# Kernel tuning notes

Hardware: AMD Instinct MI355X
Metric: run time of the kernel (lower is better)

## Reference

```python
import jax, jax.numpy as jnp
import numpy as np

E = 1024      # embed_dim
H = 16        # num_heads
HD = E // H   # head_dim = 64
WIN = 256     # window_size
LN_EPS = 1e-5


def _layernorm(x, g, b):
    mu = jnp.mean(x, axis=-1, keepdims=True)
    var = jnp.var(x, axis=-1, keepdims=True)
    return (x - mu) * jax.lax.rsqrt(var + LN_EPS) * g + b


def _rope_tables(S):
    freqs = 1.0 / (10000.0 ** (jnp.arange(0, HD, 2, dtype=jnp.float32) / HD))  # [HD/2]
    t = jnp.arange(S, dtype=jnp.float32)
    fr = jnp.outer(t, freqs)                      # [S, HD/2]
    emb = jnp.concatenate([fr, fr], axis=-1)      # [S, HD]
    # shape [S, 1, HD] so it broadcasts over the heads dim of [B, S, H, HD]
    return emb[:, None, :].astype(jnp.float32), None


def _rotate_half(x):
    x1, x2 = jnp.split(x, 2, axis=-1)
    return jnp.concatenate([-x2, x1], axis=-1)


def setup_inputs() -> dict:
    key = jax.random.key(0)
    ks = jax.random.split(key, 12)
    B, S = 8, 1024
    sc = 0.02
    return {
        "x": jax.random.normal(ks[0], (B, S, E), dtype=jnp.float32),
        "in_proj_w": jax.random.normal(ks[1], (3 * E, E), dtype=jnp.float32) * sc,
        "in_proj_b": jnp.zeros((3 * E,), dtype=jnp.float32),
        "out_proj_w": jax.random.normal(ks[2], (E, E), dtype=jnp.float32) * sc,
        "out_proj_b": jnp.zeros((E,), dtype=jnp.float32),
        "ln1_g": jnp.ones((E,), dtype=jnp.float32),
        "ln1_b": jnp.zeros((E,), dtype=jnp.float32),
        "w1": jax.random.normal(ks[3], (4 * E, E), dtype=jnp.float32) * sc,
        "b1": jnp.zeros((4 * E,), dtype=jnp.float32),
        "w2": jax.random.normal(ks[4], (E, 4 * E), dtype=jnp.float32) * sc,
        "b2": jnp.zeros((E,), dtype=jnp.float32),
        "ln2_g": jnp.ones((E,), dtype=jnp.float32),
        "ln2_b": jnp.zeros((E,), dtype=jnp.float32),
    }


def reference(x, in_proj_w, in_proj_b, out_proj_w, out_proj_b,
              ln1_g, ln1_b, w1, b1, w2, b2, ln2_g, ln2_b):
    B, S, _ = x.shape
    # RoPE applied to the raw input (pre in_proj), as in the torch module
    emb, _ = _rope_tables(S)
    cos, sin = jnp.cos(emb), jnp.sin(emb)          # [S, 1, HD]
    xh = x.reshape(B, S, H, HD)
    roped = xh * cos + _rotate_half(xh) * sin      # [B, S, H, HD]
    qk_in = roped.reshape(B, S, E)

    Wq, Wk, Wv = jnp.split(in_proj_w, 3, axis=0)   # each [E, E]
    bq, bk, bv = jnp.split(in_proj_b, 3, axis=0)
    q = (qk_in @ Wq.T + bq).reshape(B, S, H, HD).transpose(0, 2, 1, 3)  # [B,H,S,HD]
    k = (qk_in @ Wk.T + bk).reshape(B, S, H, HD).transpose(0, 2, 1, 3)
    v = (x @ Wv.T + bv).reshape(B, S, H, HD).transpose(0, 2, 1, 3)

    scale = 1.0 / np.sqrt(HD)
    scores = jnp.einsum("bhqd,bhkd->bhqk", q, k) * scale  # [B,H,S,S]
    idx = jnp.arange(S)
    disallowed = jnp.abs(idx[:, None] - idx[None, :]) > WIN  # [S,S] bool
    scores = jnp.where(disallowed, jnp.float32(-jnp.inf), scores)
    attn = jax.nn.softmax(scores, axis=-1)
    ctx = jnp.einsum("bhqk,bhkd->bhqd", attn, v)            # [B,H,S,HD]
    ctx = ctx.transpose(0, 2, 1, 3).reshape(B, S, E)
    h = ctx @ out_proj_w.T + out_proj_b

    x1 = _layernorm(x + h, ln1_g, ln1_b)
    ff = jax.nn.gelu(x1 @ w1.T + b1, approximate=False) @ w2.T + b2
    return _layernorm(x1 + ff, ln2_g, ln2_b)
```

## Files before the change

kernel.cpp:

```cpp
#include <hip/hip_runtime.h>
#include <stdint.h>


#define B_ 8
#define S_ 1024
#define E_ 1024
#define H_ 16
#define HD_ 64
#define WIN_ 256
#define QKV_ 3072

typedef __attribute__((ext_vector_type(8))) short short8;
typedef __attribute__((ext_vector_type(4))) float f32x4;
typedef __attribute__((ext_vector_type(4))) unsigned short us4;
typedef unsigned short ushort_t;

__device__ __forceinline__ ushort_t f2b(float f) {
  unsigned int u = __builtin_bit_cast(unsigned int, f);
  u = (u + 0x7fffu + ((u >> 16) & 1u)) >> 16;
  return (ushort_t)u;
}

__device__ __forceinline__ ushort_t f2b_trunc(float f) {
  return (ushort_t)(__builtin_bit_cast(unsigned int, f) >> 16);
}

__device__ __forceinline__ float b2f(ushort_t u) {
  return __builtin_bit_cast(float, ((unsigned int)u) << 16);
}

__device__ __forceinline__ float fast_exp2(float x) {
#if __has_builtin(__builtin_amdgcn_exp2f)
  return __builtin_amdgcn_exp2f(x);
#else
  return exp2f(x);
#endif
}

__device__ __forceinline__ float fast_rcp(float x) {
#if __has_builtin(__builtin_amdgcn_rcpf)
  return __builtin_amdgcn_rcpf(x);
#else
  return 1.f / x;
#endif
}

__device__ __forceinline__ void gld_lds16(const void* g, void* l) {
  __builtin_amdgcn_global_load_lds((const __attribute__((address_space(1))) void*)g,
                                   (__attribute__((address_space(3))) void*)l, 16, 0, 0);
}

__global__ __launch_bounds__(256) void cast4_kernel(const float* __restrict__ i0,
                                                    const float* __restrict__ i1,
                                                    const float* __restrict__ i2,
                                                    const float* __restrict__ i3,
                                                    ushort_t* __restrict__ o0,
                                                    ushort_t* __restrict__ o1,
                                                    ushort_t* __restrict__ o2,
                                                    ushort_t* __restrict__ o3) {
  int i = blockIdx.x * 256 + threadIdx.x;
  const float* in;
  ushort_t* out;
  int j;
  if (i < 786432)       { in = i0; out = o0; j = i; }
  else if (i < 1048576) { in = i1; out = o1; j = i - 786432; }
  else if (i < 2097152) { in = i2; out = o2; j = i - 1048576; }
  else                  { in = i3; out = o3; j = i - 2097152; }
  float4 v = ((const float4*)in)[j];
  us4 o;
  o.x = f2b(v.x); o.y = f2b(v.y); o.z = f2b(v.z); o.w = f2b(v.w);
  ((us4*)out)[j] = o;
}

__global__ __launch_bounds__(256) void rope_kernel(const float* __restrict__ x,
                                                   ushort_t* __restrict__ roped,
                                                   ushort_t* __restrict__ xbf) {
  int idx = blockIdx.x * 256 + threadIdx.x;
  int d = idx & 31;
  int h = (idx >> 5) & 15;
  int s = (idx >> 9) & 1023;
  int b = idx >> 19;
  size_t base = ((size_t)(b * S_ + s)) * E_ + h * HD_ + d;
  float x0 = x[base], x1 = x[base + 32];
  float freq = exp2f(-(float)d * 0.41524101186092029f);
  float th = (float)s * freq;
  float sn, cs;
  sincosf(th, &sn, &cs);
  roped[base]      = f2b(x0 * cs - x1 * sn);
  roped[base + 32] = f2b(x1 * cs + x0 * sn);
  xbf[base]      = f2b(x0);
  xbf[base + 32] = f2b(x1);
}

template <int MODE>
__global__ __launch_bounds__(256) void gemm_bt(const ushort_t* __restrict__ A,
                                               const ushort_t* __restrict__ A2,
                                               int nsplit,
                                               const ushort_t* __restrict__ Bm,
                                               const float* __restrict__ bias,
                                               ushort_t* __restrict__ C,
                                               int N, int K) {
  __shared__ ushort_t sA[128 * 64];
  __shared__ ushort_t sB[128 * 64];
  const int tid = threadIdx.x;
  const int lane = tid & 63;
  const int wave = tid >> 6;
  const int quad = lane >> 4;
  const int lq = lane & 15;
  const int wm = (wave & 1) * 64;
  const int wn = (wave >> 1) * 64;
  const size_t bm = (size_t)blockIdx.x * 128;
  const size_t bn = (size_t)blockIdx.y * 128;
  const ushort_t* Asel = (bn >= (size_t)nsplit) ? A2 : A;

  f32x4 acc[4][4] = {};

  const int srow = lane >> 3;
  const int skc = ((lane & 7) ^ (lane >> 3)) * 8;

  for (int k0 = 0; k0 < K; k0 += 64) {
#pragma unroll
    for (int i = 0; i < 4; i++) {
      const int r0 = wave * 32 + i * 8;
      gld_lds16(Asel + (bm + r0 + srow) * K + k0 + skc, &sA[r0 * 64]);
      gld_lds16(Bm + (bn + r0 + srow) * K + k0 + skc, &sB[r0 * 64]);
    }
    __syncthreads();

#pragma unroll
    for (int kk = 0; kk < 2; kk++) {
      const int csw = (((kk * 4) + quad) ^ (lq & 7)) * 8;
      short8 av[4], bv[4];
#pragma unroll
      for (int mt = 0; mt < 4; mt++)
        av[mt] = *(const short8*)&sA[(wm + mt * 16 + lq) * 64 + csw];
#pragma unroll
      for (int nt = 0; nt < 4; nt++)
        bv[nt] = *(const short8*)&sB[(wn + nt * 16 + lq) * 64 + csw];
#pragma unroll
      for (int mt = 0; mt < 4; mt++)
#pragma unroll
        for (int nt = 0; nt < 4; nt++)
          acc[mt][nt] = __builtin_amdgcn_mfma_f32_16x16x32_bf16(av[mt], bv[nt], acc[mt][nt], 0, 0, 0);
    }
    __syncthreads();
  }

#pragma unroll
  for (int mt = 0; mt < 4; mt++) {
#pragma unroll
    for (int nt = 0; nt < 4; nt++) {
      size_t row = bm + wm + mt * 16 + quad * 4;
      size_t col = bn + wn + nt * 16 + lq;
      float bc = bias[col];
#pragma unroll
      for (int r = 0; r < 4; r++) {
        float v = acc[mt][nt][r] + bc;
        if (MODE == 1) {
          float y = 0.7978845608028654f * (v + 0.044715f * v * v * v);
          float t = fast_exp2(y * 2.8853900817779268f);
          v = v * (t * fast_rcp(1.f + t));
        }
        C[(row + r) * N + col] = f2b(v);
      }
    }
  }
}

__global__ __launch_bounds__(256) void vtrans_kernel(const ushort_t* __restrict__ qkv,
                                                     ushort_t* __restrict__ vt) {
  __shared__ ushort_t tb[64 * 65];
  int bh = blockIdx.x >> 4;
  int st = blockIdx.x & 15;
  int b = bh >> 4, h = bh & 15;
  int s0 = st * 64;
  int tid = threadIdx.x;
  int c = tid & 63, rbase = tid >> 6;
#pragma unroll
  for (int rep = 0; rep < 16; rep++) {
    int i = rep * 4 + rbase;
    tb[c * 65 + i] = qkv[(size_t)(b * S_ + s0 + i) * QKV_ + 2048 + h * HD_ + c];
  }
  __syncthreads();
#pragma unroll
  for (int rep = 0; rep < 16; rep++) {
    int d = rep * 4 + rbase;
    vt[(size_t)((b * H_ + h) * HD_ + d) * S_ + s0 + c] = tb[d * 65 + c];
  }
}

#define SC_ 0.18033688011112042f

__global__ __launch_bounds__(256) void attn_kernel(const ushort_t* __restrict__ qkv,
                                                   const ushort_t* __restrict__ vt,
                                                   ushort_t* __restrict__ ctx) {
  __shared__ ushort_t sK[2][32 * 64];
  __shared__ ushort_t sV[2][64 * 32];
  __shared__ ushort_t sP[4][16 * 36];
  const int tid = threadIdx.x;
  const int lane = tid & 63, wave = tid >> 6;
  const int quad = lane >> 4, lq = lane & 15;
  int gid = ((blockIdx.x & 7) << 8) | (blockIdx.x >> 3);
  int qs = gid & 15;
  int h = (gid >> 4) & 15;
  int b = gid >> 8;
  int qs64 = qs * 64;
  int q0 = qs64 + wave * 16;

  const size_t qoff = (size_t)(b * S_ + q0 + lq) * QKV_ + h * HD_;
  short8 a0 = *(const short8*)&qkv[qoff + quad * 8];
  short8 a1 = *(const short8*)&qkv[qoff + 32 + quad * 8];

  f32x4 o[4] = {};
  float rs[4] = {0.f, 0.f, 0.f, 0.f};

  int start = qs64 - WIN_; if (start < 0) start = 0;
  int end = qs64 + 64 + WIN_; if (end > S_) end = S_;
  const int wlo = q0 - WIN_;
  const int whi = q0 + 16 + WIN_;

  const ushort_t* kg = qkv + (size_t)(b * S_) * QKV_ + 1024 + h * HD_;
  const ushort_t* vg = vt + (size_t)((b * H_ + h) * HD_) * S_;

  const int krow = lane >> 3;
  const int kchg = ((lane & 7) ^ krow) << 3;
  const int vrow = lane >> 2;
  const int vchg = ((lane & 3) ^ ((lane >> 3) & 3)) << 3;

  gld_lds16(kg + (size_t)(start + wave * 8 + krow) * QKV_ + kchg, &sK[0][wave * 512]);
  gld_lds16(vg + (size_t)(wave * 16 + vrow) * S_ + start + vchg, &sV[0][wave * 512]);

  const int nch = (end - start) >> 5;
  int buf = 0;
  for (int c = 0; c < nch; c++) {
    __syncthreads();
    int kb = start + c * 32;
    if (c + 1 < nch) {
      int nkb = kb + 32;
      gld_lds16(kg + (size_t)(nkb + wave * 8 + krow) * QKV_ + kchg, &sK[buf ^ 1][wave * 512]);
      gld_lds16(vg + (size_t)(wave * 16 + vrow) * S_ + nkb + vchg, &sV[buf ^ 1][wave * 512]);
    }
    if (kb < whi && kb + 32 > wlo) {
      f32x4 s[2];
#pragma unroll
      for (int t = 0; t < 2; t++) {
        const ushort_t* kr = &sK[buf][(t * 16 + lq) * 64];
        short8 b0 = *(const short8*)&kr[((quad ^ (lq & 7)) << 3)];
        short8 b1 = *(const short8*)&kr[(((4 + quad) ^ (lq & 7)) << 3)];
        f32x4 z = {};
        z = __builtin_amdgcn_mfma_f32_16x16x32_bf16(a0, b0, z, 0, 0, 0);
        z = __builtin_amdgcn_mfma_f32_16x16x32_bf16(a1, b1, z, 0, 0, 0);
        s[t] = z;
      }
      float p[2][4];
      const bool full = (kb >= q0 - 241) && (kb <= q0 + 225);
      if (full) {
#pragma unroll
        for (int t = 0; t < 2; t++)
#pragma unroll
          for (int r = 0; r < 4; r++) p[t][r] = fast_exp2(s[t][r] * SC_);
      } else {
#pragma unroll
        for (int t = 0; t < 2; t++) {
          int ki = kb + t * 16 + lq;
#pragma unroll
          for (int r = 0; r < 4; r++) {
            int dd = q0 + quad * 4 + r - ki;
            bool allowed = (dd <= WIN_) && (dd >= -WIN_);
            p[t][r] = allowed ? fast_exp2(s[t][r] * SC_) : 0.f;
          }
        }
      }
#pragma unroll
      for (int r = 0; r < 4; r++) rs[r] += p[0][r] + p[1][r];

#pragma unroll
      for (int t = 0; t < 2; t++)
#pragma unroll
        for (int r = 0; r < 4; r++)
          sP[wave][(quad * 4 + r) * 36 + t * 16 + lq] = f2b_trunc(p[t][r]);
      asm volatile("s_waitcnt lgkmcnt(0)" ::: "memory");
      short8 ap = *(const short8*)&sP[wave][lq * 36 + quad * 8];

#pragma unroll
      for (int nt = 0; nt < 4; nt++) {
        short8 bvf = *(const short8*)&sV[buf][(nt * 16 + lq) * 32 +
                                             ((quad ^ ((lq >> 1) & 3)) << 3)];
        o[nt] = __builtin_amdgcn_mfma_f32_16x16x32_bf16(ap, bvf, o[nt], 0, 0, 0);
      }
    }
    buf ^= 1;
  }

  float inv[4];
#pragma unroll
  for (int r = 0; r < 4; r++) {
    float v = rs[r];
    v += __shfl_xor(v, 1);
    v += __shfl_xor(v, 2);
    v += __shfl_xor(v, 4);
    v += __shfl_xor(v, 8);
    inv[r] = 1.f / v;
  }

#pragma unroll
  for (int nt = 0; nt < 4; nt++)
#pragma unroll
    for (int r = 0; r < 4; r++) {
      int row = q0 + quad * 4 + r;
      int col = h * HD_ + nt * 16 + lq;
      ctx[(size_t)(b * S_ + row) * E_ + col] = f2b(o[nt][r] * inv[r]);
    }
}

__global__ __launch_bounds__(256) void ln_res_kernel(const float* __restrict__ A,
                                                     const ushort_t* __restrict__ Bv,
                                                     const float* __restrict__ g,
                                                     const float* __restrict__ be,
                                                     float* __restrict__ outf,
                                                     ushort_t* __restrict__ outb) {
  const int row = blockIdx.x;
  const int tid = threadIdx.x;
  const size_t base = (size_t)row * 1024;
  float4 a4 = ((const float4*)(A + base))[tid];
  us4 b4 = ((const us4*)(Bv + base))[tid];
  float v[4];
  v[0] = a4.x + b2f(b4.x);
  v[1] = a4.y + b2f(b4.y);
  v[2] = a4.z + b2f(b4.z);
  v[3] = a4.w + b2f(b4.w);
  float s = v[0] + v[1] + v[2] + v[3];
  float sq = v[0] * v[0] + v[1] * v[1] + v[2] * v[2] + v[3] * v[3];
#pragma unroll
  for (int off = 32; off; off >>= 1) {
    s += __shfl_xor(s, off);
    sq += __shfl_xor(sq, off);
  }
  __shared__ float ls[4], lsq[4];
  int wave = tid >> 6, lane = tid & 63;
  if (lane == 0) { ls[wave] = s; lsq[wave] = sq; }
  __syncthreads();
  s = ls[0] + ls[1] + ls[2] + ls[3];
  sq = lsq[0] + lsq[1] + lsq[2] + lsq[3];
  float mean = s * (1.f / 1024.f);
  float var = sq * (1.f / 1024.f) - mean * mean;
  float rstd = rsqrtf(var + 1e-5f);
  float4 g4 = ((const float4*)g)[tid];
  float4 e4 = ((const float4*)be)[tid];
  float o0 = (v[0] - mean) * rstd * g4.x + e4.x;
  float o1 = (v[1] - mean) * rstd * g4.y + e4.y;
  float o2 = (v[2] - mean) * rstd * g4.z + e4.z;
  float o3 = (v[3] - mean) * rstd * g4.w + e4.w;
  float4 of = {o0, o1, o2, o3};
  ((float4*)(outf + base))[tid] = of;
  if (outb) {
    us4 ob;
    ob.x = f2b(o0); ob.y = f2b(o1); ob.z = f2b(o2); ob.w = f2b(o3);
    ((us4*)(outb + base))[tid] = ob;
  }
}

#define O_XBF   ((size_t)0)
#define O_ROPED ((size_t)16777216)
#define O_W_IN  ((size_t)33554432)
#define O_W_OUT ((size_t)39845888)
#define O_W1    ((size_t)41943040)
#define O_W2    ((size_t)50331648)
#define O_BIG   ((size_t)58720256)
#define O_VT    ((size_t)125829120)
#define O_X1F   ((size_t)142606336)
#define O_FF2   ((size_t)176160768)

extern "C" void kernel_launch(void* const* d_in, const int* in_sizes, int n_in,
                              void* d_out, int out_size, void* d_ws, size_t ws_size,
                              hipStream_t stream) {
  const float* x          = (const float*)d_in[0];
  const float* in_proj_w  = (const float*)d_in[1];
  const float* in_proj_b  = (const float*)d_in[2];
  const float* out_proj_w = (const float*)d_in[3];
  const float* out_proj_b = (const float*)d_in[4];
  const float* ln1_g      = (const float*)d_in[5];
  const float* ln1_b      = (const float*)d_in[6];
  const float* w1         = (const float*)d_in[7];
  const float* b1         = (const float*)d_in[8];
  const float* w2         = (const float*)d_in[9];
  const float* b2         = (const float*)d_in[10];
  const float* ln2_g      = (const float*)d_in[11];
  const float* ln2_b      = (const float*)d_in[12];
  float* out = (float*)d_out;

  char* ws = (char*)d_ws;
  ushort_t* xbf     = (ushort_t*)(ws + O_XBF);
  ushort_t* roped   = (ushort_t*)(ws + O_ROPED);
  ushort_t* wbf_in  = (ushort_t*)(ws + O_W_IN);
  ushort_t* wbf_out = (ushort_t*)(ws + O_W_OUT);
  ushort_t* wbf_1   = (ushort_t*)(ws + O_W1);
  ushort_t* wbf_2   = (ushort_t*)(ws + O_W2);
  ushort_t* qkv_buf = (ushort_t*)(ws + O_BIG);
  ushort_t* vtb     = (ushort_t*)(ws + O_VT);
  ushort_t* ctx     = (ushort_t*)(ws + O_ROPED);
  ushort_t* h_bf    = (ushort_t*)(ws + O_BIG);
  float*    x1f     = (float*)(ws + O_X1F);
  ushort_t* x1bf    = (ushort_t*)(ws + O_XBF);
  ushort_t* ff1     = (ushort_t*)(ws + O_BIG);
  ushort_t* ff2     = (ushort_t*)(ws + O_FF2);

  dim3 blk(256);
  const int NOSPLIT = 1 << 30;

  cast4_kernel<<<dim3(12288), blk, 0, stream>>>(in_proj_w, out_proj_w, w1, w2,
                                                wbf_in, wbf_out, wbf_1, wbf_2);

  rope_kernel<<<dim3(16384), blk, 0, stream>>>(x, roped, xbf);

  gemm_bt<0><<<dim3(64, 24), blk, 0, stream>>>(roped, xbf, 2048, wbf_in, in_proj_b,
                                               qkv_buf, QKV_, 1024);
  vtrans_kernel<<<dim3(2048), blk, 0, stream>>>(qkv_buf, vtb);

  attn_kernel<<<dim3(2048), blk, 0, stream>>>(qkv_buf, vtb, ctx);

  gemm_bt<0><<<dim3(64, 8), blk, 0, stream>>>(ctx, ctx, NOSPLIT, wbf_out, out_proj_b,
                                              h_bf, 1024, 1024);

  ln_res_kernel<<<dim3(8192), blk, 0, stream>>>(x, h_bf, ln1_g, ln1_b, x1f, x1bf);

  gemm_bt<1><<<dim3(64, 32), blk, 0, stream>>>(x1bf, x1bf, NOSPLIT, wbf_1, b1,
                                               ff1, 4096, 1024);

  gemm_bt<0><<<dim3(64, 8), blk, 0, stream>>>(ff1, ff1, NOSPLIT, wbf_2, b2,
                                              ff2, 1024, 4096);

  ln_res_kernel<<<dim3(8192), blk, 0, stream>>>(x1f, ff2, ln2_g, ln2_b, out, nullptr);
}
```

Baseline: 473.6 us.

## Keep attention probabilities in registers via transposed QK MFMA; remap GEMM block order

Swaps the operands of the QK^T MFMA so each lane holds score values laid out as the A operand of the PV MFMA. This lets probabilities be packed to bf16 in registers instead of round-tripping through a per-wave LDS scratch buffer with a waitcnt. The V fragment reads are adjusted to match the new key ordering, and the row sum becomes a single scalar per lane combined with cross-quad shuffles and a fast reciprocal. Separately, the GEMMs move to a 1D grid with a swizzled block mapping, intended to improve L2 reuse across the M dimension.

```diff
diff --git a/kernel.cpp b/kernel.cpp
--- a/kernel.cpp
+++ b/kernel.cpp
@@ -13,16 +13,13 @@
 typedef __attribute__((ext_vector_type(8))) short short8;
 typedef __attribute__((ext_vector_type(4))) float f32x4;
 typedef __attribute__((ext_vector_type(4))) unsigned short us4;
+typedef __attribute__((ext_vector_type(4))) unsigned int u32x4;
 typedef unsigned short ushort_t;
 
 __device__ __forceinline__ ushort_t f2b(float f) {
   unsigned int u = __builtin_bit_cast(unsigned int, f);
   u = (u + 0x7fffu + ((u >> 16) & 1u)) >> 16;
   return (ushort_t)u;
-}
-
-__device__ __forceinline__ ushort_t f2b_trunc(float f) {
-  return (ushort_t)(__builtin_bit_cast(unsigned int, f) >> 16);
 }
 
 __device__ __forceinline__ float b2f(ushort_t u) {
@@ -109,8 +106,11 @@
   const int lq = lane & 15;
   const int wm = (wave & 1) * 64;
   const int wn = (wave >> 1) * 64;
-  const size_t bm = (size_t)blockIdx.x * 128;
-  const size_t bn = (size_t)blockIdx.y * 128;
+  const int bid = blockIdx.x;
+  const int bx = ((bid & 7) << 3) | ((bid >> 3) & 7);
+  const int by = bid >> 6;
+  const size_t bm = (size_t)bx * 128;
+  const size_t bn = (size_t)by * 128;
   const ushort_t* Asel = (bn >= (size_t)nsplit) ? A2 : A;
 
   f32x4 acc[4][4] = {};
@@ -196,7 +196,6 @@
                                                    ushort_t* __restrict__ ctx) {
   __shared__ ushort_t sK[2][32 * 64];
   __shared__ ushort_t sV[2][64 * 32];
-  __shared__ ushort_t sP[4][16 * 36];
   const int tid = threadIdx.x;
   const int lane = tid & 63, wave = tid >> 6;
   const int quad = lane >> 4, lq = lane & 15;
@@ -212,7 +211,7 @@
   short8 a1 = *(const short8*)&qkv[qoff + 32 + quad * 8];
 
   f32x4 o[4] = {};
-  float rs[4] = {0.f, 0.f, 0.f, 0.f};
+  float rs = 0.f;
 
   int start = qs64 - WIN_; if (start < 0) start = 0;
   int end = qs64 + 64 + WIN_; if (end > S_) end = S_;
@@ -232,6 +231,8 @@
 
   const int nch = (end - start) >> 5;
   int buf = 0;
+  const int r3 = (lq >> 1) & 3;
+  const int qi = q0 + lq;
   for (int c = 0; c < nch; c++) {
     __syncthreads();
     int kb = start + c * 32;
@@ -248,8 +249,8 @@
         short8 b0 = *(const short8*)&kr[((quad ^ (lq & 7)) << 3)];
         short8 b1 = *(const short8*)&kr[(((4 + quad) ^ (lq & 7)) << 3)];
         f32x4 z = {};
-        z = __builtin_amdgcn_mfma_f32_16x16x32_bf16(a0, b0, z, 0, 0, 0);
-        z = __builtin_amdgcn_mfma_f32_16x16x32_bf16(a1, b1, z, 0, 0, 0);
+        z = __builtin_amdgcn_mfma_f32_16x16x32_bf16(b0, a0, z, 0, 0, 0);
+        z = __builtin_amdgcn_mfma_f32_16x16x32_bf16(b1, a1, z, 0, 0, 0);
         s[t] = z;
       }
       float p[2][4];
@@ -262,46 +263,54 @@
       } else {
 #pragma unroll
         for (int t = 0; t < 2; t++) {
-          int ki = kb + t * 16 + lq;
+          int kbase_t = kb + t * 16 + quad * 4;
 #pragma unroll
           for (int r = 0; r < 4; r++) {
-            int dd = q0 + quad * 4 + r - ki;
+            int dd = qi - (kbase_t + r);
             bool allowed = (dd <= WIN_) && (dd >= -WIN_);
             p[t][r] = allowed ? fast_exp2(s[t][r] * SC_) : 0.f;
           }
         }
       }
-#pragma unroll
-      for (int r = 0; r < 4; r++) rs[r] += p[0][r] + p[1][r];
-
-#pragma unroll
-      for (int t = 0; t < 2; t++)
-#pragma unroll
-        for (int r = 0; r < 4; r++)
-          sP[wave][(quad * 4 + r) * 36 + t * 16 + lq] = f2b_trunc(p[t][r]);
-      asm volatile("s_waitcnt lgkmcnt(0)" ::: "memory");
-      short8 ap = *(const short8*)&sP[wave][lq * 36 + quad * 8];
+      rs += p[0][0] + p[0][1] + p[0][2] + p[0][3] +
+            p[1][0] + p[1][1] + p[1][2] + p[1][3];
+
+      u32x4 pk;
+      {
+        unsigned int u00 = __builtin_bit_cast(unsigned int, p[0][0]);
+        unsigned int u01 = __builtin_bit_cast(unsigned int, p[0][1]);
+        unsigned int u02 = __builtin_bit_cast(unsigned int, p[0][2]);
+        unsigned int u03 = __builtin_bit_cast(unsigned int, p[0][3]);
+        unsigned int u10 = __builtin_bit_cast(unsigned int, p[1][0]);
+        unsigned int u11 = __builtin_bit_cast(unsigned int, p[1][1]);
+        unsigned int u12 = __builtin_bit_cast(unsigned int, p[1][2]);
+        unsigned int u13 = __builtin_bit_cast(unsigned int, p[1][3]);
+        pk.x = (u01 & 0xFFFF0000u) | (u00 >> 16);
+        pk.y = (u03 & 0xFFFF0000u) | (u02 >> 16);
+        pk.z = (u11 & 0xFFFF0000u) | (u10 >> 16);
+        pk.w = (u13 & 0xFFFF0000u) | (u12 >> 16);
+      }
+      short8 ap = __builtin_bit_cast(short8, pk);
 
 #pragma unroll
       for (int nt = 0; nt < 4; nt++) {
-        short8 bvf = *(const short8*)&sV[buf][(nt * 16 + lq) * 32 +
-                                             ((quad ^ ((lq >> 1) & 3)) << 3)];
+        const uint2* vrow2 = (const uint2*)&sV[buf][(nt * 16 + lq) * 32];
+        uint2 lo = vrow2[(((quad >> 1)) ^ r3) * 2 + (quad & 1)];
+        uint2 hi = vrow2[(((quad >> 1) + 2) ^ r3) * 2 + (quad & 1)];
+        u32x4 vv; vv.x = lo.x; vv.y = lo.y; vv.z = hi.x; vv.w = hi.y;
+        short8 bvf = __builtin_bit_cast(short8, vv);
         o[nt] = __builtin_amdgcn_mfma_f32_16x16x32_bf16(ap, bvf, o[nt], 0, 0, 0);
       }
     }
     buf ^= 1;
   }
 
+  rs += __shfl_xor(rs, 16);
+  rs += __shfl_xor(rs, 32);
   float inv[4];
 #pragma unroll
-  for (int r = 0; r < 4; r++) {
-    float v = rs[r];
-    v += __shfl_xor(v, 1);
-    v += __shfl_xor(v, 2);
-    v += __shfl_xor(v, 4);
-    v += __shfl_xor(v, 8);
-    inv[r] = 1.f / v;
-  }
+  for (int r = 0; r < 4; r++)
+    inv[r] = fast_rcp(__shfl(rs, quad * 4 + r));
 
 #pragma unroll
   for (int nt = 0; nt < 4; nt++)
@@ -413,22 +422,22 @@
 
   rope_kernel<<<dim3(16384), blk, 0, stream>>>(x, roped, xbf);
 
-  gemm_bt<0><<<dim3(64, 24), blk, 0, stream>>>(roped, xbf, 2048, wbf_in, in_proj_b,
-                                               qkv_buf, QKV_, 1024);
+  gemm_bt<0><<<dim3(64 * 24), blk, 0, stream>>>(roped, xbf, 2048, wbf_in, in_proj_b,
+                                                qkv_buf, QKV_, 1024);
   vtrans_kernel<<<dim3(2048), blk, 0, stream>>>(qkv_buf, vtb);
 
   attn_kernel<<<dim3(2048), blk, 0, stream>>>(qkv_buf, vtb, ctx);
 
-  gemm_bt<0><<<dim3(64, 8), blk, 0, stream>>>(ctx, ctx, NOSPLIT, wbf_out, out_proj_b,
-                                              h_bf, 1024, 1024);
+  gemm_bt<0><<<dim3(64 * 8), blk, 0, stream>>>(ctx, ctx, NOSPLIT, wbf_out, out_proj_b,
+                                               h_bf, 1024, 1024);
 
   ln_res_kernel<<<dim3(8192), blk, 0, stream>>>(x, h_bf, ln1_g, ln1_b, x1f, x1bf);
 
-  gemm_bt<1><<<dim3(64, 32), blk, 0, stream>>>(x1bf, x1bf, NOSPLIT, wbf_1, b1,
-                                               ff1, 4096, 1024);
-
-  gemm_bt<0><<<dim3(64, 8), blk, 0, stream>>>(ff1, ff1, NOSPLIT, wbf_2, b2,
-                                              ff2, 1024, 4096);
+  gemm_bt<1><<<dim3(64 * 32), blk, 0, stream>>>(x1bf, x1bf, NOSPLIT, wbf_1, b1,
+                                                ff1, 4096, 1024);
+
+  gemm_bt<0><<<dim3(64 * 8), blk, 0, stream>>>(ff1, ff1, NOSPLIT, wbf_2, b2,
+                                               ff2, 1024, 4096);
 
   ln_res_kernel<<<dim3(8192), blk, 0, stream>>>(x1f, ff2, ln2_g, ln2_b, out, nullptr);
 }
```

After: 479.0 us. No clear change (+1.1%).
